# Performance work log

Hardware: AMD Instinct MI355X
Metric: run time of the kernel (lower is better)

## Reference

```python
import jax, jax.numpy as jnp
import numpy as np

B, D, V = 1024, 512, 100000
M = 0.4
EPS = 1e-07


def setup_inputs() -> dict:
    key = jax.random.key(0)
    k1, k2, k3 = jax.random.split(key, 3)
    inp = jax.random.normal(k1, (B, D), dtype=jnp.float32)
    # xavier_uniform for (D, V): limit = sqrt(6/(D+V))
    limit = float(np.sqrt(6.0 / (D + V)))
    weight = jax.random.uniform(k2, (D, V), dtype=jnp.float32, minval=-limit, maxval=limit)
    labels = jax.random.randint(k3, (B,), 0, V, dtype=jnp.int64)
    return {"input": inp, "weight": weight, "labels": labels}


def reference(input, weight, labels):
    # L2-normalize rows of input and columns of weight (F.normalize eps=1e-12)
    x_norm = input / jnp.maximum(jnp.linalg.norm(input, axis=1, keepdims=True), 1e-12)
    w_norm = weight / jnp.maximum(jnp.linalg.norm(weight, axis=0, keepdims=True), 1e-12)
    cosine = x_norm @ w_norm                                # [B, V]
    cosine = jnp.clip(cosine, -1.0 + EPS, 1.0 - EPS)
    arcos = jnp.arccos(cosine)
    # add margin m only at the label class (one-hot add without dense one-hot)
    rows = jnp.arange(B)
    arcos = arcos.at[rows, labels].add(M)
    logits = jnp.cos(arcos)                                 # [B, V]
    # cross-entropy, mean reduction
    logz = jax.nn.logsumexp(logits, axis=1)                 # [B]
    label_logit = logits[rows, labels]                      # [B]
    loss = jnp.mean(logz - label_logit)
    return loss
```

## Files before the change

kernel.cpp:

```cpp
#include <hip/hip_runtime.h>
#include <hip/hip_bf16.h>
#include <math.h>

#define B_    1024
#define D_    512
#define V_    100000
#define NT_   782
#define EPS_  1e-7f
#define COSM  0.9210609940028851f
#define SINM  0.3894183423086505f

typedef __bf16 bf16x8 __attribute__((ext_vector_type(8)));
typedef float  f32x4  __attribute__((ext_vector_type(4)));

struct alignas(16) US8 { unsigned short h[8]; };

__device__ __forceinline__ unsigned short f2bf(float f) {
  union { float f; unsigned u; } a; a.f = f;
  unsigned u = a.u;
  u += 0x7FFFu + ((u >> 16) & 1u);
  return (unsigned short)(u >> 16);
}

__device__ __forceinline__ void async_copy16(void* lds, const void* g) {
  __builtin_amdgcn_global_load_lds(
      (const __attribute__((address_space(1))) void*)g,
      (__attribute__((address_space(3))) void*)lds, 16, 0, 0);
}

__global__ void x_prep(const float* __restrict__ x,
                       unsigned short* __restrict__ xb,
                       float* __restrict__ S) {
  int t = threadIdx.x;
  int lane = t & 63, wave = t >> 6;
  int row = blockIdx.x * 4 + wave;
  const float* xr = x + (size_t)row * D_;
  f32x4 a = *(const f32x4*)(xr + lane * 8);
  f32x4 b = *(const f32x4*)(xr + lane * 8 + 4);
  float ss = a[0]*a[0] + a[1]*a[1] + a[2]*a[2] + a[3]*a[3]
           + b[0]*b[0] + b[1]*b[1] + b[2]*b[2] + b[3]*b[3];
#pragma unroll
  for (int off = 32; off > 0; off >>= 1) ss += __shfl_xor(ss, off, 64);
  float inv = 1.0f / fmaxf(sqrtf(ss), 1e-12f);
  US8 pk;
#pragma unroll
  for (int j = 0; j < 4; ++j) pk.h[j]     = f2bf(a[j] * inv);
#pragma unroll
  for (int j = 0; j < 4; ++j) pk.h[4 + j] = f2bf(b[j] * inv);
  *(US8*)(xb + (size_t)row * D_ + lane * 8) = pk;
  if (lane == 0) S[row] = 0.0f;
}

#define BM 128
#define BN 128
#define BK 64

__global__ __launch_bounds__(256) void gemm_fused(
    const unsigned short* __restrict__ xb,
    const float* __restrict__ w,
    const int* __restrict__ labels,
    float* __restrict__ S, float* __restrict__ Lb) {
  int bid = blockIdx.x;
  int xcd = bid & 7;
  int slot = bid >> 3;
  int tn = xcd * 98 + (slot >> 3);
  int tm = slot & 7;
  if (tn >= NT_) return;
  int m0 = tm * BM, n0 = tn * BN;

  __shared__ unsigned short Ab[BM * BK];
  __shared__ unsigned short Bb[BN * BK];
  __shared__ float sqred[8][BN];
  __shared__ float iwL[BN];
  __shared__ int labT[BM];
  int t = threadIdx.x;
  if (t < BM) labT[t] = labels[m0 + t];
  int lane = t & 63;
  int q = lane >> 4, l15 = lane & 15;
  int wave = t >> 6;
  int wm = (wave & 1) * 64, wn = (wave >> 1) * 64;
  f32x4 acc[4][4] = {};

  const unsigned short* gA[4];
  unsigned short* lA[4];
#pragma unroll
  for (int j = 0; j < 4; ++j) {
    int p = t + 256 * j;
    int m = p >> 3;
    int kc = (p & 7) ^ (m & 7);
    gA[j] = xb + (size_t)(m0 + m) * D_ + kc * 8;
    lA[j] = Ab + p * 8;
  }

  int cg = t & 31;
  int rp = t >> 5;
  int c0l = cg * 4;
  bool vok = (n0 + c0l + 3) < V_;
  const float* wbase = w + (size_t)rp * 8 * V_ + n0 + c0l;
  unsigned short* bdst[4];
#pragma unroll
  for (int cc = 0; cc < 4; ++cc) {
    int col = c0l + cc;
    bdst[cc] = &Bb[(col * 8 + (rp ^ (col & 7))) * 8];
  }
  float ssq[4] = {0.0f, 0.0f, 0.0f, 0.0f};

  for (int kt = 0; kt < D_; kt += BK) {
#pragma unroll
    for (int j = 0; j < 4; ++j) async_copy16(lA[j], gA[j] + kt);

    f32x4 row[8];
    if (vok) {
#pragma unroll
      for (int i = 0; i < 8; ++i)
        row[i] = *(const f32x4*)(wbase + (size_t)i * V_);
    } else {
#pragma unroll
      for (int i = 0; i < 8; ++i) row[i] = f32x4{0.0f, 0.0f, 0.0f, 0.0f};
    }
#pragma unroll
    for (int cc = 0; cc < 4; ++cc) {
      US8 pk;
#pragma unroll
      for (int i = 0; i < 8; ++i) {
        float v = row[i][cc];
        ssq[cc] += v * v;
        pk.h[i] = f2bf(v);
      }
      *(US8*)bdst[cc] = pk;
    }
    wbase += (size_t)BK * V_;

    __syncthreads();
    int h = l15 & 7;
#pragma unroll
    for (int s = 0; s < 2; ++s) {
      int kx = s * 4 + q;
      bf16x8 af[4], bfr[4];
#pragma unroll
      for (int ri = 0; ri < 4; ++ri) {
        int row_ = wm + ri * 16 + l15;
        af[ri] = *(const bf16x8*)&Ab[(row_ * 8 + (kx ^ h)) * 8];
      }
#pragma unroll
      for (int ci = 0; ci < 4; ++ci) {
        int row_ = wn + ci * 16 + l15;
        bfr[ci] = *(const bf16x8*)&Bb[(row_ * 8 + (kx ^ h)) * 8];
      }
#pragma unroll
      for (int ri = 0; ri < 4; ++ri)
#pragma unroll
        for (int ci = 0; ci < 4; ++ci)
          acc[ri][ci] = __builtin_amdgcn_mfma_f32_16x16x32_bf16(
              af[ri], bfr[ci], acc[ri][ci], 0, 0, 0);
    }
    __syncthreads();
  }

#pragma unroll
  for (int cc = 0; cc < 4; ++cc) sqred[rp][c0l + cc] = ssq[cc];
  __syncthreads();
  if (t < BN) {
    float tot = 0.0f;
#pragma unroll
    for (int p = 0; p < 8; ++p) tot += sqred[p][t];
    iwL[t] = ((n0 + t) < V_) ? 1.0f / fmaxf(sqrtf(tot), 1e-12f) : 0.0f;
  }
  __syncthreads();

  float iw[4]; int vcol[4];
#pragma unroll
  for (int ci = 0; ci < 4; ++ci) {
    int nl = wn + ci * 16 + l15;
    vcol[ci] = n0 + nl;
    iw[ci] = iwL[nl];
  }
#pragma unroll
  for (int ri = 0; ri < 4; ++ri) {
#pragma unroll
    for (int reg = 0; reg < 4; ++reg) {
      int ml = wm + ri * 16 + q * 4 + reg;
      int r = m0 + ml;
      int lab = labT[ml];
      float s = 0.0f;
#pragma unroll
      for (int ci = 0; ci < 4; ++ci) {
        float cv = acc[ri][ci][reg] * iw[ci];
        cv = fminf(fmaxf(cv, -1.0f + EPS_), 1.0f - EPS_);
        float logit = cv;
        if (vcol[ci] == lab) {
          logit = cv * COSM - sqrtf(fmaxf(1.0f - cv * cv, 0.0f)) * SINM;
          Lb[r] = logit;
        }
        s += (vcol[ci] < V_) ? __expf(logit) : 0.0f;
      }
      s += __shfl_xor(s, 1, 64);
      s += __shfl_xor(s, 2, 64);
      s += __shfl_xor(s, 4, 64);
      s += __shfl_xor(s, 8, 64);
      if (l15 == 0) atomicAdd(&S[r], s);
    }
  }
}

__global__ void finalk(const float* __restrict__ S, const float* __restrict__ Lb,
                       float* __restrict__ out) {
  __shared__ float red[256];
  int t = threadIdx.x;
  float s = 0.0f;
  for (int i = t; i < B_; i += 256) s += logf(S[i]) - Lb[i];
  red[t] = s;
  __syncthreads();
  for (int o = 128; o > 0; o >>= 1) {
    if (t < o) red[t] += red[t + o];
    __syncthreads();
  }
  if (t == 0) out[0] = red[0] * (1.0f / B_);
}

extern "C" void kernel_launch(void* const* d_in, const int* in_sizes, int n_in,
                              void* d_out, int out_size, void* d_ws, size_t ws_size,
                              hipStream_t stream) {
  const float* x = (const float*)d_in[0];
  const float* w = (const float*)d_in[1];
  const int* labels = (const int*)d_in[2];
  float* out = (float*)d_out;
  char* ws = (char*)d_ws;
  unsigned short* xb = (unsigned short*)ws;
  float* S  = (float*)(ws + 1048576ull);
  float* Lb = (float*)(ws + 1052672ull);

  x_prep<<<256, 256, 0, stream>>>(x, xb, S);
  gemm_fused<<<6272, 256, 0, stream>>>(xb, w, labels, S, Lb);
  finalk<<<1, 256, 0, stream>>>(S, Lb, out);
}
```

Measured before the change: 518.6 us.

## Precompute transposed bf16 weights and column norms, then use async DMA GEMM

Adds a w_prep pass that reads the fp32 weight once, writes a transposed bf16 copy padded to the tile width, and accumulates per-column sums of squares with atomics. The GEMM then loads both operands straight into LDS with async global-to-LDS copies instead of converting fp32 weights in registers. This removes the repeated fp32 reads and conversions done by each of the 8 row tiles sharing a column tile. The cost is an extra pass, about 100MB of workspace traffic, and a fallback to the old kernel when the workspace is too small.

```diff
diff --git a/kernel.cpp b/kernel.cpp
--- a/kernel.cpp
+++ b/kernel.cpp
@@ -1,10 +1,10 @@
 #include <hip/hip_runtime.h>
-#include <hip/hip_bf16.h>
 #include <math.h>
 
 #define B_    1024
 #define D_    512
 #define V_    100000
+#define NP_   100096
 #define NT_   782
 #define EPS_  1e-7f
 #define COSM  0.9210609940028851f
@@ -51,11 +51,153 @@
   if (lane == 0) S[row] = 0.0f;
 }
 
+__global__ __launch_bounds__(256) void w_prep(const float* __restrict__ w,
+                                              unsigned short* __restrict__ wbT,
+                                              float* __restrict__ wssq) {
+  int t  = threadIdx.x;
+  int c0 = blockIdx.x * 1024 + t * 4;
+  int r0 = blockIdx.y * 64;
+  bool valid = (c0 + 3) < V_;
+  if (valid) {
+    const float* src = w + (size_t)r0 * V_ + c0;
+    float ssq[4] = {0.0f, 0.0f, 0.0f, 0.0f};
+    for (int rr = 0; rr < 64; rr += 8) {
+      US8 out[4];
+#pragma unroll
+      for (int i = 0; i < 8; ++i) {
+        f32x4 v = *(const f32x4*)(src + (size_t)(rr + i) * V_);
+#pragma unroll
+        for (int cc = 0; cc < 4; ++cc) {
+          ssq[cc] += v[cc] * v[cc];
+          out[cc].h[i] = f2bf(v[cc]);
+        }
+      }
+#pragma unroll
+      for (int cc = 0; cc < 4; ++cc)
+        *(US8*)(wbT + (size_t)(c0 + cc) * D_ + r0 + rr) = out[cc];
+    }
+#pragma unroll
+    for (int cc = 0; cc < 4; ++cc) atomicAdd(&wssq[c0 + cc], ssq[cc]);
+  } else if (c0 < NP_) {
+    US8 z = {};
+    for (int rr = 0; rr < 64; rr += 8)
+#pragma unroll
+      for (int cc = 0; cc < 4; ++cc)
+        *(US8*)(wbT + (size_t)(c0 + cc) * D_ + r0 + rr) = z;
+  }
+}
+
 #define BM 128
 #define BN 128
 #define BK 64
 
-__global__ __launch_bounds__(256) void gemm_fused(
+__global__ __launch_bounds__(256) void gemm_fused_dma(
+    const unsigned short* __restrict__ xb,
+    const unsigned short* __restrict__ wbT,
+    const float* __restrict__ wssq,
+    const int* __restrict__ labels,
+    float* __restrict__ S, float* __restrict__ Lb) {
+  int bid = blockIdx.x;
+  int xcd = bid & 7;
+  int slot = bid >> 3;
+  int tn = xcd * 98 + (slot >> 3);
+  int tm = slot & 7;
+  if (tn >= NT_) return;
+  int m0 = tm * BM, n0 = tn * BN;
+
+  __shared__ unsigned short Ab[BM * BK];
+  __shared__ unsigned short Bb[BN * BK];
+  __shared__ int labT[BM];
+  int t = threadIdx.x;
+  if (t < BM) labT[t] = labels[m0 + t];
+  int lane = t & 63;
+  int q = lane >> 4, l15 = lane & 15;
+  int wave = t >> 6;
+  int wm = (wave & 1) * 64, wn = (wave >> 1) * 64;
+  f32x4 acc[4][4] = {};
+
+  const unsigned short* gA[4]; unsigned short* lA[4];
+  const unsigned short* gB[4]; unsigned short* lB[4];
+#pragma unroll
+  for (int j = 0; j < 4; ++j) {
+    int p = t + 256 * j;
+    int m = p >> 3;
+    int kc = (p & 7) ^ (m & 7);
+    gA[j] = xb  + (size_t)(m0 + m) * D_ + kc * 8;
+    lA[j] = Ab + p * 8;
+    gB[j] = wbT + (size_t)(n0 + m) * D_ + kc * 8;
+    lB[j] = Bb + p * 8;
+  }
+
+  for (int kt = 0; kt < D_; kt += BK) {
+#pragma unroll
+    for (int j = 0; j < 4; ++j) async_copy16(lA[j], gA[j] + kt);
+#pragma unroll
+    for (int j = 0; j < 4; ++j) async_copy16(lB[j], gB[j] + kt);
+    __syncthreads();
+
+    int h = l15 & 7;
+#pragma unroll
+    for (int s = 0; s < 2; ++s) {
+      int kx = s * 4 + q;
+      bf16x8 af[4], bfr[4];
+#pragma unroll
+      for (int ri = 0; ri < 4; ++ri) {
+        int row_ = wm + ri * 16 + l15;
+        af[ri] = *(const bf16x8*)&Ab[(row_ * 8 + (kx ^ h)) * 8];
+      }
+#pragma unroll
+      for (int ci = 0; ci < 4; ++ci) {
+        int row_ = wn + ci * 16 + l15;
+        bfr[ci] = *(const bf16x8*)&Bb[(row_ * 8 + (kx ^ h)) * 8];
+      }
+#pragma unroll
+      for (int ri = 0; ri < 4; ++ri)
+#pragma unroll
+        for (int ci = 0; ci < 4; ++ci)
+          acc[ri][ci] = __builtin_amdgcn_mfma_f32_16x16x32_bf16(
+              af[ri], bfr[ci], acc[ri][ci], 0, 0, 0);
+    }
+    __syncthreads();
+  }
+
+  float iw[4]; int vcol[4];
+#pragma unroll
+  for (int ci = 0; ci < 4; ++ci) {
+    int nl = wn + ci * 16 + l15;
+    vcol[ci] = n0 + nl;
+    iw[ci] = (vcol[ci] < V_) ? 1.0f / fmaxf(sqrtf(wssq[vcol[ci]]), 1e-12f)
+                             : 0.0f;
+  }
+#pragma unroll
+  for (int ri = 0; ri < 4; ++ri) {
+#pragma unroll
+    for (int reg = 0; reg < 4; ++reg) {
+      int ml = wm + ri * 16 + q * 4 + reg;
+      int r = m0 + ml;
+      int lab = labT[ml];
+      float s = 0.0f;
+#pragma unroll
+      for (int ci = 0; ci < 4; ++ci) {
+        float cv = acc[ri][ci][reg] * iw[ci];
+        cv = fminf(fmaxf(cv, -1.0f + EPS_), 1.0f - EPS_);
+        float logit = cv;
+        if (vcol[ci] == lab) {
+          logit = cv * COSM - sqrtf(fmaxf(1.0f - cv * cv, 0.0f)) * SINM;
+          Lb[r] = logit;
+        }
+        s += (vcol[ci] < V_) ? __expf(logit) : 0.0f;
+      }
+      s += __shfl_xor(s, 1, 64);
+      s += __shfl_xor(s, 2, 64);
+      s += __shfl_xor(s, 4, 64);
+      s += __shfl_xor(s, 8, 64);
+      if (l15 == 0) atomicAdd(&S[r], s);
+    }
+  }
+}
+
+__global__ __launch_bounds__(256) void gemm_fused_inline(
     const unsigned short* __restrict__ xb,
     const float* __restrict__ w,
     const int* __restrict__ labels,
@@ -227,10 +369,19 @@
   float* out = (float*)d_out;
   char* ws = (char*)d_ws;
   unsigned short* xb = (unsigned short*)ws;
-  float* S  = (float*)(ws + 1048576ull);
-  float* Lb = (float*)(ws + 1052672ull);
+  float* S    = (float*)(ws + 1048576ull);
+  float* Lb   = (float*)(ws + 1052672ull);
+  float* wssq = (float*)(ws + 1056768ull);
+  unsigned short* wbT = (unsigned short*)(ws + 1457152ull);
+  const size_t WS_NEED = 1457152ull + (size_t)NP_ * D_ * 2ull;
 
   x_prep<<<256, 256, 0, stream>>>(x, xb, S);
-  gemm_fused<<<6272, 256, 0, stream>>>(xb, w, labels, S, Lb);
+  if (ws_size >= WS_NEED) {
+    hipMemsetAsync(wssq, 0, (size_t)NP_ * sizeof(float), stream);
+    w_prep<<<dim3(98, 8), 256, 0, stream>>>(w, wbT, wssq);
+    gemm_fused_dma<<<6272, 256, 0, stream>>>(xb, wbT, wssq, labels, S, Lb);
+  } else {
+    gemm_fused_inline<<<6272, 256, 0, stream>>>(xb, w, labels, S, Lb);
+  }
   finalk<<<1, 256, 0, stream>>>(S, Lb, out);
 }
```

After: 622.3 us. +20.0%, slower.

## Enlarge GEMM M-tile to 512 with 1024-thread blocks and register-prefetch weights

Applied to the files above, without the earlier changes.

Raises the M tile from 128 to 512 rows with 16 waves per block, so each fp32 weight tile is read from global memory and converted to bf16 by 2 blocks instead of 8. This cuts redundant weight traffic and conversion work. Weight loads are now prefetched into registers one K-step ahead to overlap them with the MFMA work. In exchange, the larger blocks lower scheduling flexibility and occupancy, and each thread now reads its label straight from global memory.

```diff
diff --git a/kernel.cpp b/kernel.cpp
--- a/kernel.cpp
+++ b/kernel.cpp
@@ -1,5 +1,4 @@
 #include <hip/hip_runtime.h>
-#include <hip/hip_bf16.h>
 #include <math.h>
 
 #define B_    1024
@@ -51,11 +50,12 @@
   if (lane == 0) S[row] = 0.0f;
 }
 
-#define BM 128
+#define BM 512
 #define BN 128
 #define BK 64
-
-__global__ __launch_bounds__(256) void gemm_fused(
+#define NKT (D_ / BK)
+
+__global__ __launch_bounds__(1024) void gemm_fused(
     const unsigned short* __restrict__ xb,
     const float* __restrict__ w,
     const int* __restrict__ labels,
@@ -63,8 +63,8 @@
   int bid = blockIdx.x;
   int xcd = bid & 7;
   int slot = bid >> 3;
-  int tn = xcd * 98 + (slot >> 3);
-  int tm = slot & 7;
+  int tm = slot & 1;
+  int tn = xcd * 98 + (slot >> 1);
   if (tn >= NT_) return;
   int m0 = tm * BM, n0 = tn * BN;
 
@@ -72,67 +72,63 @@
   __shared__ unsigned short Bb[BN * BK];
   __shared__ float sqred[8][BN];
   __shared__ float iwL[BN];
-  __shared__ int labT[BM];
   int t = threadIdx.x;
-  if (t < BM) labT[t] = labels[m0 + t];
   int lane = t & 63;
   int q = lane >> 4, l15 = lane & 15;
   int wave = t >> 6;
-  int wm = (wave & 1) * 64, wn = (wave >> 1) * 64;
+  int wm = (wave & 7) * 64, wn = (wave >> 3) * 64;
   f32x4 acc[4][4] = {};
 
-  const unsigned short* gA[4];
-  unsigned short* lA[4];
+  const unsigned short* gA[4]; unsigned short* lA[4];
 #pragma unroll
   for (int j = 0; j < 4; ++j) {
-    int p = t + 256 * j;
+    int p = t + 1024 * j;
     int m = p >> 3;
     int kc = (p & 7) ^ (m & 7);
     gA[j] = xb + (size_t)(m0 + m) * D_ + kc * 8;
     lA[j] = Ab + p * 8;
   }
 
-  int cg = t & 31;
-  int rp = t >> 5;
-  int c0l = cg * 4;
-  bool vok = (n0 + c0l + 3) < V_;
-  const float* wbase = w + (size_t)rp * 8 * V_ + n0 + c0l;
-  unsigned short* bdst[4];
-#pragma unroll
-  for (int cc = 0; cc < 4; ++cc) {
-    int col = c0l + cc;
-    bdst[cc] = &Bb[(col * 8 + (rp ^ (col & 7))) * 8];
-  }
-  float ssq[4] = {0.0f, 0.0f, 0.0f, 0.0f};
-
-  for (int kt = 0; kt < D_; kt += BK) {
+  int col = t & 127;
+  int kc8 = t >> 7;
+  bool vok = (n0 + col) < V_;
+  const float* wc = w + (size_t)(kc8 * 8) * V_ + n0 + col;
+  unsigned short* bdst = &Bb[(col * 8 + (kc8 ^ (col & 7))) * 8];
+  float ssq = 0.0f;
+
+  float breg[8];
+  if (vok) {
+#pragma unroll
+    for (int i = 0; i < 8; ++i) breg[i] = wc[(size_t)i * V_];
+  } else {
+#pragma unroll
+    for (int i = 0; i < 8; ++i) breg[i] = 0.0f;
+  }
+
+  int h = l15 & 7;
+  for (int tt = 0; tt < NKT; ++tt) {
+    int kt = tt * BK;
 #pragma unroll
     for (int j = 0; j < 4; ++j) async_copy16(lA[j], gA[j] + kt);
 
-    f32x4 row[8];
-    if (vok) {
-#pragma unroll
-      for (int i = 0; i < 8; ++i)
-        row[i] = *(const f32x4*)(wbase + (size_t)i * V_);
-    } else {
-#pragma unroll
-      for (int i = 0; i < 8; ++i) row[i] = f32x4{0.0f, 0.0f, 0.0f, 0.0f};
-    }
-#pragma unroll
-    for (int cc = 0; cc < 4; ++cc) {
-      US8 pk;
-#pragma unroll
-      for (int i = 0; i < 8; ++i) {
-        float v = row[i][cc];
-        ssq[cc] += v * v;
-        pk.h[i] = f2bf(v);
-      }
-      *(US8*)bdst[cc] = pk;
-    }
-    wbase += (size_t)BK * V_;
-
+    US8 pk;
+#pragma unroll
+    for (int i = 0; i < 8; ++i) {
+      float v = breg[i];
+      ssq += v * v;
+      pk.h[i] = f2bf(v);
+    }
+    *(US8*)bdst = pk;
     __syncthreads();
-    int h = l15 & 7;
+
+    if (tt + 1 < NKT) {
+      const float* wn_ = wc + (size_t)(kt + BK) * V_;
+      if (vok) {
+#pragma unroll
+        for (int i = 0; i < 8; ++i) breg[i] = wn_[(size_t)i * V_];
+      }
+    }
+
 #pragma unroll
     for (int s = 0; s < 2; ++s) {
       int kx = s * 4 + q;
@@ -157,8 +153,7 @@
     __syncthreads();
   }
 
-#pragma unroll
-  for (int cc = 0; cc < 4; ++cc) sqred[rp][c0l + cc] = ssq[cc];
+  sqred[kc8][col] = ssq;
   __syncthreads();
   if (t < BN) {
     float tot = 0.0f;
@@ -181,7 +176,7 @@
     for (int reg = 0; reg < 4; ++reg) {
       int ml = wm + ri * 16 + q * 4 + reg;
       int r = m0 + ml;
-      int lab = labT[ml];
+      int lab = labels[r];
       float s = 0.0f;
 #pragma unroll
       for (int ci = 0; ci < 4; ++ci) {
@@ -231,6 +226,6 @@
   float* Lb = (float*)(ws + 1052672ull);
 
   x_prep<<<256, 256, 0, stream>>>(x, xb, S);
-  gemm_fused<<<6272, 256, 0, stream>>>(xb, w, labels, S, Lb);
+  gemm_fused<<<1568, 1024, 0, stream>>>(xb, w, labels, S, Lb);
   finalk<<<1, 256, 0, stream>>>(S, Lb, out);
 }
```

Result: slower. 702.8 us (+35.5%).
